# Optimization experiments

Measured on AMD Instinct MI355X. Metric: run time of the kernel, lower is better.

## Reference

```python
import jax, jax.numpy as jnp
import numpy as np

B, N, H = 8, 2000, 64  # batch, num_nodes(=input_dim), hidden(num_gru_units)


def _laplacian_self_loop(a):
    # batched: norm = D^{-1/2} (A + I) D^{-1/2}
    m = a + jnp.eye(a.shape[-1], dtype=a.dtype)
    d_inv_sqrt = jnp.sum(m, axis=-1) ** -0.5  # (B, N)
    return d_inv_sqrt[..., :, None] * m * d_inv_sqrt[..., None, :]


def _graph_conv(inputs, hidden_flat, adj, windd, W2, b2, W3, b3, W, b, out_dim):
    b_, _, n = inputs.shape
    # dynamic wind-based adjacency
    wind_now = inputs[:, 2, :] * 360.0  # (B, N)
    direction = jnp.abs(windd[None, :, :] - wind_now[:, :, None])  # (B, N, N)
    direction = jnp.where(direction > 360.0, 180.0, direction)
    d1 = jnp.maximum(jnp.cos(direction * (jnp.pi / 180.0)), 0.0)
    a = d1 @ W2.T + b2 + (adj @ W3.T + b3)[None]  # (B, N, N)
    a1 = _laplacian_self_loop(jnp.maximum(a, 0.0))
    # graph conv: concat [x, h] then A @ [.] then Linear
    x = jnp.concatenate([inputs[:, 0, :, None], hidden_flat.reshape(b_, n, H)], axis=2)  # (B,N,H+1)
    y = jnp.einsum('bij,bjh->bih', a1, x) @ W.T + b  # (B, N, out_dim)
    return y.reshape(b_, n * out_dim)


def reference(inputs, hidden_state, adj, windd, W2, b2, W3, b3, W1a, b1a, W1b, b1b, Wca1, Wca2, Wsa):
    b_, _, n = inputs.shape
    conc = _graph_conv(inputs, hidden_state, adj, windd, W2, b2, W3, b3, W1a, b1a, 2 * H)
    conc = conc.reshape(b_, 2 * H, n)  # faithful reshape (input_dim == N)
    # --- channel attention (CBAM) ---
    avg = jnp.mean(conc, axis=2, keepdims=True)  # (B, 2H, 1)
    mx = jnp.max(conc, axis=2, keepdims=True)
    def fc(v):
        return jnp.einsum('oc,bcx->box', Wca2, jax.nn.relu(jnp.einsum('oc,bcx->box', Wca1, v)))
    ca = jax.nn.sigmoid(fc(avg) + fc(mx))  # (B, 2H, 1)
    conc = ca * conc
    # --- spatial attention ---
    s = jnp.stack([jnp.mean(conc, axis=1), jnp.max(conc, axis=1)], axis=1)  # (B, 2, N)
    sa = jax.lax.conv_general_dilated(s, Wsa, window_strides=(1,), padding=((3, 3),),
                                      dimension_numbers=('NCH', 'OIH', 'NCH'))  # (B,1,N)
    conc = jax.nn.sigmoid(sa) * conc
    # --- GRU gates ---
    conc = jax.nn.sigmoid(conc.reshape(b_, 2 * H * n))
    r, u = jnp.split(conc, 2, axis=1)  # each (B, N*H)
    c = jnp.tanh(_graph_conv(inputs, r * hidden_state, adj, windd, W2, b2, W3, b3, W1b, b1b, H))
    new_hidden_state = u * hidden_state + (1.0 - u) * c
    return new_hidden_state


def setup_inputs() -> dict:
    key = jax.random.key(0)
    ks = jax.random.split(key, 12)
    inputs = jax.random.uniform(ks[0], (B, 3, N), dtype=jnp.float32)
    hidden_state = jax.random.normal(ks[1], (B, N * H), dtype=jnp.float32) * 0.1
    adj = jax.random.uniform(ks[2], (N, N), dtype=jnp.float32)
    windd = jax.random.uniform(ks[3], (N, N), dtype=jnp.float32) * 360.0
    sN = 1.0 / np.sqrt(N)
    W2 = jax.random.normal(ks[4], (N, N), dtype=jnp.float32) * sN
    b2 = jnp.zeros((N,), jnp.float32)
    W3 = jax.random.normal(ks[5], (N, N), dtype=jnp.float32) * sN
    b3 = jnp.zeros((N,), jnp.float32)
    sI = 1.0 / np.sqrt(H + 1)
    W1a = jax.random.normal(ks[6], (2 * H, H + 1), dtype=jnp.float32) * sI
    b1a = jnp.ones((2 * H,), jnp.float32)  # bias=1.0 in graph_conv1
    W1b = jax.random.normal(ks[7], (H, H + 1), dtype=jnp.float32) * sI
    b1b = jnp.zeros((H,), jnp.float32)
    Wca1 = jax.random.normal(ks[8], (2 * H // 16, 2 * H), dtype=jnp.float32) * (1.0 / np.sqrt(2 * H))
    Wca2 = jax.random.normal(ks[9], (2 * H, 2 * H // 16), dtype=jnp.float32) * (1.0 / np.sqrt(2 * H // 16))
    Wsa = jax.random.normal(ks[10], (1, 2, 7), dtype=jnp.float32) * (1.0 / np.sqrt(14))
    return {'inputs': inputs, 'hidden_state': hidden_state, 'adj': adj, 'windd': windd,
            'W2': W2, 'b2': b2, 'W3': W3, 'b3': b3, 'W1a': W1a, 'b1a': b1a,
            'W1b': W1b, 'b1b': b1b, 'Wca1': Wca1, 'Wca2': Wca2, 'Wsa': Wsa}
```

## Files before the change

kernel.cpp:

```cpp
#include <hip/hip_runtime.h>

#define NN 2000
#define BB 8
#define P  2048
#define NIT 32

typedef __attribute__((ext_vector_type(8))) short bf16x8;
typedef __attribute__((ext_vector_type(4))) float f32x4;

__device__ __forceinline__ float sigf(float x) { return 1.0f / (1.0f + expf(-x)); }

__device__ __forceinline__ short f2bf(float x) {
    union { float f; unsigned u; } v; v.f = x;
    unsigned r = v.u + 0x7fffu + ((v.u >> 16) & 1u);
    return (short)(r >> 16);
}
__device__ __forceinline__ float bf2f(short h) {
    union { unsigned u; float f; } v; v.u = ((unsigned)(unsigned short)h) << 16; return v.f;
}

__device__ __forceinline__ void gl2lds16(const short* g, short* l) {
    __builtin_amdgcn_global_load_lds(
        (const __attribute__((address_space(1))) void*)g,
        (__attribute__((address_space(3))) void*)l, 16, 0, 0);
}

__global__ __launch_bounds__(256) void k_cvt(
    const float* __restrict__ W2, const float* __restrict__ W3,
    const float* __restrict__ adj, const float* __restrict__ windd,
    const float* __restrict__ inputs,
    short* __restrict__ W2bf, short* __restrict__ W3bf,
    short* __restrict__ adjbf, short* __restrict__ d1bf)
{
    const int i = blockIdx.x, sel = blockIdx.y, t = threadIdx.x;
    const bool live = (i < NN) && (t < 250);
    if (sel < 3) {
        const float* s = (sel == 0) ? W2 : (sel == 1) ? W3 : adj;
        short* d = ((sel == 0) ? W2bf : (sel == 1) ? W3bf : adjbf) + ((size_t)i) * P + t * 8;
        bf16x8 v;
#pragma unroll
        for (int e = 0; e < 8; ++e) v[e] = 0;
        if (live) {
            const float* p = s + (size_t)i * NN + t * 8;
            float4 x0 = *(const float4*)p;
            float4 x1 = *(const float4*)(p + 4);
            float a[8] = {x0.x,x0.y,x0.z,x0.w,x1.x,x1.y,x1.z,x1.w};
#pragma unroll
            for (int e = 0; e < 8; ++e) v[e] = f2bf(a[e]);
        }
        *(bf16x8*)d = v;
    } else {
        const float DEG = 0.01745329251994329577f;
        float cw[8], sw[8];
        if (live) {
            const float* p = windd + (size_t)i * NN + t * 8;
            float4 x0 = *(const float4*)p;
            float4 x1 = *(const float4*)(p + 4);
            float a[8] = {x0.x,x0.y,x0.z,x0.w,x1.x,x1.y,x1.z,x1.w};
#pragma unroll
            for (int e = 0; e < 8; ++e) {
                float r = a[e] * DEG;
                cw[e] = __cosf(r);
                sw[e] = __sinf(r);
            }
        }
        __shared__ float cwn[8], swn[8];
        if (t < 8 && i < NN) {
            float wn = inputs[(size_t)t * 3 * NN + 2 * NN + i] * (360.0f * DEG);
            cwn[t] = __cosf(wn);
            swn[t] = __sinf(wn);
        }
        __syncthreads();
#pragma unroll
        for (int b = 0; b < BB; ++b) {
            bf16x8 v;
#pragma unroll
            for (int e = 0; e < 8; ++e) v[e] = 0;
            if (live) {
                const float cb_ = cwn[b], sb_ = swn[b];
#pragma unroll
                for (int e = 0; e < 8; ++e)
                    v[e] = f2bf(fmaxf(fmaf(cw[e], cb_, sw[e] * sb_), 0.0f));
            }
            *(bf16x8*)(d1bf + ((size_t)b * P + i) * P + t * 8) = v;
        }
    }
}

__global__ __launch_bounds__(512, 2) void k_gd(
    const short* __restrict__ d1bf, const short* __restrict__ W2bf,
    const float* __restrict__ b2, const short* __restrict__ adjw,
    short* __restrict__ m_bf, float* __restrict__ rowpart)
{
    __shared__ char smem[131072];
    const int t = threadIdx.x;
    const int w = t >> 6, lane = t & 63;
    const int wm = w >> 2, wn = w & 3;
    const int lr = lane & 15, lq = lane >> 4;
    const int tile = blockIdx.x;
    const int b = blockIdx.y;
    const int i0 = (tile & 7) * 256;
    const int j0 = (tile >> 3) * 256;
    const short* A  = d1bf + (size_t)b * P * P;
    const short* Bm = W2bf;

    const short* srcA[4];
    const short* srcB[4];
#pragma unroll
    for (int q = 0; q < 4; ++q) {
        const int c = q * 512 + t;
        const int r = c >> 3;
        const int g = (c & 7) ^ (r & 7);
        srcA[q] = A  + (size_t)(i0 + r) * P + g * 8;
        srcB[q] = Bm + (size_t)(j0 + r) * P + g * 8;
    }

#define STAGE_ALL(slot, ktI) do {                                                      \
        gl2lds16(srcA[0] + (ktI) * 64, (short*)(smem + (slot) * 32768 + (w * 64) * 16));          \
        gl2lds16(srcA[1] + (ktI) * 64, (short*)(smem + (slot) * 32768 + (512 + w * 64) * 16));    \
        gl2lds16(srcA[2] + (ktI) * 64, (short*)(smem + (slot) * 32768 + (1024 + w * 64) * 16));   \
        gl2lds16(srcA[3] + (ktI) * 64, (short*)(smem + (slot) * 32768 + (1536 + w * 64) * 16));   \
        gl2lds16(srcB[0] + (ktI) * 64, (short*)(smem + 65536 + (slot) * 32768 + (w * 64) * 16));          \
        gl2lds16(srcB[1] + (ktI) * 64, (short*)(smem + 65536 + (slot) * 32768 + (512 + w * 64) * 16));    \
        gl2lds16(srcB[2] + (ktI) * 64, (short*)(smem + 65536 + (slot) * 32768 + (1024 + w * 64) * 16));   \
        gl2lds16(srcB[3] + (ktI) * 64, (short*)(smem + 65536 + (slot) * 32768 + (1536 + w * 64) * 16)); } while (0)

    const int fx0 = (lq << 4) ^ ((lr & 7) << 4);
    const int fx1 = ((4 + lq) << 4) ^ ((lr & 7) << 4);
    const int arowB = (wm * 128 + lr) * 128;
    const int browB = (wn * 64 + lr) * 128;

    f32x4 acc[8][4];
#pragma unroll
    for (int m = 0; m < 8; ++m)
#pragma unroll
        for (int n = 0; n < 4; ++n) acc[m][n] = (f32x4){0.f, 0.f, 0.f, 0.f};
    bf16x8 aF[4][2], bF[4][2];

    STAGE_ALL(0, 0);
    asm volatile("s_waitcnt vmcnt(0)" ::: "memory");
    __builtin_amdgcn_s_barrier();
    asm volatile("" ::: "memory");

#define MFMA_(a_, b_, m, n) acc[m][n] = __builtin_amdgcn_mfma_f32_16x16x32_bf16(a_, b_, acc[m][n], 0, 0, 0)

    for (int kt = 0; kt < NIT; ++kt) {
        char* curA = smem + (kt & 1) * 32768;
        char* curB = smem + 65536 + (kt & 1) * 32768;
        const int stgSlot = (kt + 1) & 1;
        const int stgKt = (kt + 1 < NIT) ? (kt + 1) : (NIT - 1);

        STAGE_ALL(stgSlot, stgKt);

#pragma unroll
        for (int m = 0; m < 4; ++m) {
            aF[m][0] = *(const bf16x8*)(curA + arowB + m * 2048 + fx0);
            aF[m][1] = *(const bf16x8*)(curA + arowB + m * 2048 + fx1);
        }
#pragma unroll
        for (int n = 0; n < 4; ++n) {
            bF[n][0] = *(const bf16x8*)(curB + browB + n * 2048 + fx0);
            bF[n][1] = *(const bf16x8*)(curB + browB + n * 2048 + fx1);
        }
        asm volatile("s_waitcnt lgkmcnt(0)" ::: "memory");
        __builtin_amdgcn_sched_barrier(0);
        __builtin_amdgcn_s_setprio(1);
#pragma unroll
        for (int m = 0; m < 4; ++m)
#pragma unroll
            for (int n = 0; n < 4; ++n) {
                MFMA_(aF[m][0], bF[n][0], m, n);
                MFMA_(aF[m][1], bF[n][1], m, n);
            }
        __builtin_amdgcn_s_setprio(0);

#pragma unroll
        for (int m = 0; m < 4; ++m) {
            aF[m][0] = *(const bf16x8*)(curA + arowB + (m + 4) * 2048 + fx0);
            aF[m][1] = *(const bf16x8*)(curA + arowB + (m + 4) * 2048 + fx1);
        }
        asm volatile("s_waitcnt lgkmcnt(0)" ::: "memory");
        __builtin_amdgcn_sched_barrier(0);
        __builtin_amdgcn_s_setprio(1);
#pragma unroll
        for (int m = 0; m < 4; ++m)
#pragma unroll
            for (int n = 0; n < 4; ++n) {
                MFMA_(aF[m][0], bF[n][0], m + 4, n);
                MFMA_(aF[m][1], bF[n][1], m + 4, n);
            }
        __builtin_amdgcn_s_setprio(0);

        asm volatile("s_waitcnt vmcnt(0)" ::: "memory");
        __builtin_amdgcn_s_barrier();
        asm volatile("" ::: "memory");
    }

    const int rbase = i0 + wm * 128 + lq * 4;
    const int cbase = j0 + wn * 64 + lr;
    float* red = (float*)smem;
#pragma unroll
    for (int m = 0; m < 8; ++m) {
#pragma unroll
        for (int q = 0; q < 4; ++q) {
            const int row = rbase + m * 16 + q;
            float rs = 0.0f;
#pragma unroll
            for (int n = 0; n < 4; ++n) {
                const int col = cbase + n * 16;
                short o = 0;
                if (row < NN && col < NN) {
                    float x = acc[m][n][q] + b2[col] + bf2f(adjw[(size_t)row * NN + col]);
                    x = fmaxf(x, 0.0f);
                    if (row == col) x += 1.0f;
                    o = f2bf(x);
                    rs += x;
                }
                m_bf[((size_t)b * P + row) * P + col] = o;
            }
            red[(wm * 128 + m * 16 + lq * 4 + q) * 66 + (wn * 16 + lr)] = rs;
        }
    }
    __syncthreads();
    if (t < 256) {
        const float* rr = red + t * 66;
        float s = 0.0f;
#pragma unroll
        for (int k2 = 0; k2 < 64; ++k2) s += rr[k2];
        const int row = i0 + t;
        if (row < NN)
            rowpart[((size_t)b * 8 + (tile >> 3)) * 2048 + row] = s;
    }
#undef MFMA_
#undef STAGE_ALL
}

template<int EPI, int OUTD>
__global__ __launch_bounds__(256) void k_mfma(
    const short* __restrict__ Abase, const short* __restrict__ Bbase,
    const float* __restrict__ bias, const short* __restrict__ adjw,
    void* __restrict__ Cout, short* __restrict__ part, size_t aBatch)
{
    __shared__ short shA[4096];
    __shared__ short shB[4096];
    const int t = threadIdx.x;
    const int w = t >> 6, lane = t & 63;
    const int wr = w >> 1, wc = w & 1;

    int i0, j0, b, kt = 0;
    if (EPI == 2) {
        i0 = blockIdx.x * 128; j0 = 0; kt = blockIdx.y; b = blockIdx.z;
    } else {
        i0 = blockIdx.x * 128; j0 = blockIdx.y * 128; b = 0;
    }
    const int kb = (EPI == 2) ? kt * (P / 4) : 0;
    const int ke = (EPI == 2) ? kt * (P / 4) + (P / 4) : P;

    const short* A  = Abase + (size_t)b * aBatch;
    const short* Bm = Bbase + ((EPI == 2) ? (size_t)b * 128 * P : (size_t)0);

    f32x4 acc[4][4];
#pragma unroll
    for (int m = 0; m < 4; ++m)
#pragma unroll
        for (int n = 0; n < 4; ++n) acc[m][n] = (f32x4){0.f, 0.f, 0.f, 0.f};

    const int lidx0 = w * 128 + lane;
    const int lidx1 = lidx0 + 64;
    const short* aS0 = A  + (size_t)(i0 + (lidx0 >> 2)) * P + (lidx0 & 3) * 8;
    const short* aS1 = A  + (size_t)(i0 + (lidx1 >> 2)) * P + (lidx1 & 3) * 8;
    const short* bS0 = Bm + (size_t)(j0 + (lidx0 >> 2)) * P + (lidx0 & 3) * 8;
    const short* bS1 = Bm + (size_t)(j0 + (lidx1 >> 2)) * P + (lidx1 & 3) * 8;
    short* ldA0 = shA + (w * 128) * 8;
    short* ldA1 = shA + (w * 128 + 64) * 8;
    short* ldB0 = shB + (w * 128) * 8;
    short* ldB1 = shB + (w * 128 + 64) * 8;

    const int lr = lane & 15, lq = lane >> 4;
    const int aoff = (wr * 64 + lr) * 32 + lq * 8;
    const int boff = (wc * 64 + lr) * 32 + lq * 8;

    for (int k0 = kb; k0 < ke; k0 += 32) {
        gl2lds16(aS0 + k0, ldA0);
        gl2lds16(aS1 + k0, ldA1);
        gl2lds16(bS0 + k0, ldB0);
        gl2lds16(bS1 + k0, ldB1);
        __syncthreads();
        bf16x8 aF[4], bF[4];
#pragma unroll
        for (int m = 0; m < 4; ++m) aF[m] = *(const bf16x8*)(shA + aoff + m * 512);
#pragma unroll
        for (int n = 0; n < 4; ++n) bF[n] = *(const bf16x8*)(shB + boff + n * 512);
#pragma unroll
        for (int m = 0; m < 4; ++m)
#pragma unroll
            for (int n = 0; n < 4; ++n)
                acc[m][n] = __builtin_amdgcn_mfma_f32_16x16x32_bf16(aF[m], bF[n], acc[m][n], 0, 0, 0);
        __syncthreads();
    }

    const int rbase = i0 + wr * 64 + lq * 4;
    const int cbase = j0 + wc * 64 + lr;
#pragma unroll
    for (int m = 0; m < 4; ++m) {
#pragma unroll
        for (int n = 0; n < 4; ++n) {
            const int col = cbase + n * 16;
#pragma unroll
            for (int q = 0; q < 4; ++q) {
                const int row = rbase + m * 16 + q;
                float v = acc[m][n][q];
                if (EPI == 0) {
                    if (row < NN && col < NN)
                        ((short*)Cout)[(size_t)row * NN + col] = f2bf(v + bias[col]);
                } else {
                    if (row < NN && col < OUTD)
                        part[((size_t)(kt * BB + b) * NN + row) * OUTD + col] = f2bf(v);
                }
            }
        }
    }
}

__global__ __launch_bounds__(256) void k_combred(
    const short* __restrict__ part, const float* __restrict__ dinv,
    const float* __restrict__ bias, float* __restrict__ conc,
    float* __restrict__ avg, float* __restrict__ mx)
{
    const int c = blockIdx.x, b = blockIdx.y, t = threadIdx.x;
    const size_t S = (size_t)BB * NN * 128;
    const size_t base = (size_t)b * NN * 128;
    float sm = 0.0f, sx = -3.402823466e+38f;
    for (int n = t; n < NN; n += 256) {
        const size_t f = (size_t)c * NN + n;
        const int i = (int)(f >> 7), o = (int)(f & 127);
        const size_t pidx = base + f;
        float s = (bf2f(part[pidx]) + bf2f(part[pidx + S])) +
                  (bf2f(part[pidx + 2 * S]) + bf2f(part[pidx + 3 * S]));
        float v = s * dinv[b * NN + i] + bias[o];
        conc[pidx] = v;
        sm += v; sx = fmaxf(sx, v);
    }
#pragma unroll
    for (int off = 32; off > 0; off >>= 1) {
        sm += __shfl_down(sm, off);
        sx = fmaxf(sx, __shfl_down(sx, off));
    }
    __shared__ float rs[4], rm[4];
    if ((t & 63) == 0) { rs[t >> 6] = sm; rm[t >> 6] = sx; }
    __syncthreads();
    if (t == 0) {
        avg[b * 128 + c] = (rs[0] + rs[1] + rs[2] + rs[3]) * (1.0f / NN);
        mx[b * 128 + c]  = fmaxf(fmaxf(rm[0], rm[1]), fmaxf(rm[2], rm[3]));
    }
}

__global__ __launch_bounds__(256) void k_cfin(
    const short* __restrict__ part, const float* __restrict__ dinv,
    const float* __restrict__ bias, const float* __restrict__ u,
    const float* __restrict__ hidden, float* __restrict__ out)
{
    const size_t idx = (size_t)blockIdx.x * 256 + threadIdx.x;
    const size_t S = (size_t)BB * NN * 64;
    if (idx >= S) return;
    const int o = (int)(idx & 63);
    const size_t r = idx >> 6;
    const int i = (int)(r % NN);
    const int b = (int)(r / NN);
    float s = (bf2f(part[idx]) + bf2f(part[idx + S])) +
              (bf2f(part[idx + 2 * S]) + bf2f(part[idx + 3 * S]));
    float c = tanhf(s * dinv[b * NN + i] + bias[o]);
    float uu = u[idx];
    out[idx] = uu * hidden[idx] + (1.0f - uu) * c;
}

template<int OUT>
__global__ __launch_bounds__(128) void k_xwT(
    const float* __restrict__ inputs, const float* __restrict__ hsrc,
    const float* __restrict__ W, const float* __restrict__ rowpart,
    float* __restrict__ dinv, short* __restrict__ zT)
{
    const int b = blockIdx.y;
    const int j0 = blockIdx.x * 16;
    const int t = threadIdx.x;
    __shared__ float wl[128 * 65];
    __shared__ float xs[16 * 66];
    __shared__ float dj[16];
    for (int idx = t; idx < OUT * 65; idx += 128) wl[idx] = W[idx];
    for (int idx = t; idx < 16 * 64; idx += 128) {
        int jj = idx >> 6, hh = idx & 63, j = j0 + jj;
        xs[jj * 66 + 1 + hh] = (j < NN) ? hsrc[((size_t)b * NN + j) * 64 + hh] : 0.0f;
    }
    if (t < 16) {
        int j = j0 + t;
        xs[t * 66] = (j < NN) ? inputs[(size_t)b * 3 * NN + j] : 0.0f;
        float dv = 0.0f;
        if (j < NN) {
            if (OUT == 128) {
                float s = 0.0f;
#pragma unroll
                for (int jt = 0; jt < 8; ++jt)
                    s += rowpart[((size_t)b * 8 + jt) * 2048 + j];
                dv = rsqrtf(s);
                dinv[b * NN + j] = dv;
            } else {
                dv = dinv[b * NN + j];
            }
        }
        dj[t] = dv;
    }
    __syncthreads();
    for (int jj = 0; jj < 16; ++jj) {
        float a = 0.0f;
        if (t < OUT) {
            const float* xr = &xs[jj * 66];
            const float* wr = &wl[t * 65];
#pragma unroll
            for (int c = 0; c < 65; ++c) a = fmaf(xr[c], wr[c], a);
        }
        int j = j0 + jj;
        zT[((size_t)b * 128 + t) * P + j] = (t < OUT && j < NN) ? f2bf(a * dj[jj]) : (short)0;
    }
}

__global__ __launch_bounds__(256) void k_satgate(
    const float* __restrict__ conc, const float* __restrict__ avg,
    const float* __restrict__ mxv, const float* __restrict__ Wca1,
    const float* __restrict__ Wca2, const float* __restrict__ Wsa,
    const float* __restrict__ hidden, float* __restrict__ rh, float* __restrict__ u)
{
    const int b = blockIdx.y;
    const int n0 = blockIdx.x * 256;
    const int t = threadIdx.x;
    __shared__ float av[128], mv[128], h[16], cas[128];
    __shared__ float wsa[14];
    __shared__ float s0l[262], s1l[262];
    if (t < 128) { av[t] = avg[b * 128 + t]; mv[t] = mxv[b * 128 + t]; }
    if (t >= 128 && t < 142) wsa[t - 128] = Wsa[t - 128];
    __syncthreads();
    if (t < 16) {
        int o8 = t & 7;
        const float* src = (t < 8) ? av : mv;
        float s = 0.0f;
        for (int c = 0; c < 128; ++c) s = fmaf(Wca1[o8 * 128 + c], src[c], s);
        h[t] = fmaxf(s, 0.0f);
    }
    __syncthreads();
    if (t < 128) {
        float s = 0.0f;
#pragma unroll
        for (int k = 0; k < 8; ++k) s = fmaf(Wca2[t * 8 + k], h[k] + h[8 + k], s);
        cas[t] = sigf(s);
    }
    __syncthreads();

    const float* cb = conc + (size_t)b * NN * 128;
    {
        const int n = n0 + t;
        float sm = 0.0f, sx = -3.402823466e+38f;
        if (n < NN) {
            for (int c = 0; c < 128; ++c) {
                float v = cas[c] * cb[(size_t)c * NN + n];
                sm += v; sx = fmaxf(sx, v);
            }
            s0l[t + 3] = sm * (1.0f / 128.0f);
            s1l[t + 3] = sx;
        } else { s0l[t + 3] = 0.0f; s1l[t + 3] = 0.0f; }
    }
    if (t < 6) {
        const int hn = (t < 3) ? (n0 - 3 + t) : (n0 + 256 + (t - 3));
        const int hi = (t < 3) ? t : (256 + t);
        float sm = 0.0f, sx = -3.402823466e+38f;
        if (hn >= 0 && hn < NN) {
            for (int c = 0; c < 128; ++c) {
                float v = cas[c] * cb[(size_t)c * NN + hn];
                sm += v; sx = fmaxf(sx, v);
            }
            s0l[hi] = sm * (1.0f / 128.0f);
            s1l[hi] = sx;
        } else { s0l[hi] = 0.0f; s1l[hi] = 0.0f; }
    }
    __syncthreads();

    const int n = n0 + t;
    if (n >= NN) return;
    float sa = 0.0f;
#pragma unroll
    for (int k = 0; k < 7; ++k)
        sa += wsa[k] * s0l[t + k] + wsa[7 + k] * s1l[t + k];
    float gs = sigf(sa);
    for (int c = 0; c < 128; ++c) {
        float v = gs * cas[c] * cb[(size_t)c * NN + n];
        float g = sigf(v);
        if (c < 64)
            rh[(size_t)b * NN * 64 + (size_t)c * NN + n] =
                g * hidden[(size_t)b * NN * 64 + (size_t)c * NN + n];
        else
            u[(size_t)b * NN * 64 + (size_t)(c - 64) * NN + n] = g;
    }
}

extern "C" void kernel_launch(void* const* d_in, const int* in_sizes, int n_in,
                              void* d_out, int out_size, void* d_ws, size_t ws_size,
                              hipStream_t stream)
{
    (void)in_sizes; (void)n_in; (void)out_size; (void)ws_size;
    const float* inputs = (const float*)d_in[0];
    const float* hidden = (const float*)d_in[1];
    const float* adj    = (const float*)d_in[2];
    const float* windd  = (const float*)d_in[3];
    const float* W2     = (const float*)d_in[4];
    const float* b2     = (const float*)d_in[5];
    const float* W3     = (const float*)d_in[6];
    const float* b3     = (const float*)d_in[7];
    const float* W1a    = (const float*)d_in[8];
    const float* b1a    = (const float*)d_in[9];
    const float* W1b    = (const float*)d_in[10];
    const float* b1b    = (const float*)d_in[11];
    const float* Wca1   = (const float*)d_in[12];
    const float* Wca2   = (const float*)d_in[13];
    const float* Wsa    = (const float*)d_in[14];
    float* out = (float*)d_out;

    char* W = (char*)d_ws;
    short* adjW3bf = (short*)(W + 0);
    short* W2bf    = (short*)(W + 8000000);
    short* W3bf    = (short*)(W + 16388608);
    short* adjbf   = (short*)(W + 24777216);
    short* m_bf    = (short*)(W + 16388608);
    char* D = W + 83497472;
    short* d1bf = (short*)D;
    float* dinv = (float*)(D + 0);
    float* avgb = (float*)(D + 64000);
    float* mxb  = (float*)(D + 68096);
    short* zT   = (short*)(D + 204800);
    float* conc = (float*)(D + 4399104);
    float* rh   = (float*)(D + 12591104);
    float* ubuf = (float*)(D + 16687104);
    short* part = (short*)(D + 24879104);
    float* rowpart = (float*)(D + 67108864);

    const size_t PP = (size_t)P * P;

    k_cvt<<<dim3(P, 4), 256, 0, stream>>>(W2, W3, adj, windd, inputs,
                                          W2bf, W3bf, adjbf, d1bf);
    k_mfma<0, 0><<<dim3(16, 16, 1), 256, 0, stream>>>(adjbf, W3bf, b3, nullptr, adjW3bf, nullptr, 0);
    k_gd<<<dim3(64, BB), 512, 0, stream>>>(d1bf, W2bf, b2, adjW3bf, m_bf, rowpart);
    k_xwT<128><<<dim3(128, BB), 128, 0, stream>>>(inputs, hidden, W1a, rowpart, dinv, zT);
    k_mfma<2, 128><<<dim3(16, 4, BB), 256, 0, stream>>>(m_bf, zT, nullptr, nullptr, nullptr, part, PP);
    k_combred<<<dim3(128, BB), 256, 0, stream>>>(part, dinv, b1a, conc, avgb, mxb);
    k_satgate<<<dim3(8, BB), 256, 0, stream>>>(conc, avgb, mxb, Wca1, Wca2, Wsa, hidden, rh, ubuf);
    k_xwT<64><<<dim3(128, BB), 128, 0, stream>>>(inputs, rh, W1b, rowpart, dinv, zT);
    k_mfma<2, 64><<<dim3(16, 4, BB), 256, 0, stream>>>(m_bf, zT, nullptr, nullptr, nullptr, part, PP);
    k_cfin<<<(BB * NN * 64 + 255) / 256, 256, 0, stream>>>(part, dinv, b1b, ubuf, hidden, out);
}
```

Measured before the change: 396.5 us.

## Swizzle LDS layout in MFMA GEMM and add dedicated 64-wide aggregation kernel

```diff
diff --git a/kernel.cpp b/kernel.cpp
--- a/kernel.cpp
+++ b/kernel.cpp
@@ -235,10 +235,10 @@
 #undef STAGE_ALL
 }
 
-template<int EPI, int OUTD>
+template<int EPI>
 __global__ __launch_bounds__(256) void k_mfma(
     const short* __restrict__ Abase, const short* __restrict__ Bbase,
-    const float* __restrict__ bias, const short* __restrict__ adjw,
+    const float* __restrict__ bias,
     void* __restrict__ Cout, short* __restrict__ part, size_t aBatch)
 {
     __shared__ short shA[4096];
@@ -267,18 +267,22 @@
 
     const int lidx0 = w * 128 + lane;
     const int lidx1 = lidx0 + 64;
-    const short* aS0 = A  + (size_t)(i0 + (lidx0 >> 2)) * P + (lidx0 & 3) * 8;
-    const short* aS1 = A  + (size_t)(i0 + (lidx1 >> 2)) * P + (lidx1 & 3) * 8;
-    const short* bS0 = Bm + (size_t)(j0 + (lidx0 >> 2)) * P + (lidx0 & 3) * 8;
-    const short* bS1 = Bm + (size_t)(j0 + (lidx1 >> 2)) * P + (lidx1 & 3) * 8;
-    short* ldA0 = shA + (w * 128) * 8;
-    short* ldA1 = shA + (w * 128 + 64) * 8;
-    short* ldB0 = shB + (w * 128) * 8;
-    short* ldB1 = shB + (w * 128 + 64) * 8;
+    const int rA0 = lidx0 >> 2, rA1 = lidx1 >> 2;
+    const int gA0 = (lidx0 & 3) ^ ((lidx0 >> 3) & 3);
+    const int gA1 = (lidx1 & 3) ^ ((lidx1 >> 3) & 3);
+    const short* aS0 = A  + (size_t)(i0 + rA0) * P + gA0 * 8;
+    const short* aS1 = A  + (size_t)(i0 + rA1) * P + gA1 * 8;
+    const short* bS0 = Bm + (size_t)(j0 + rA0) * P + gA0 * 8;
+    const short* bS1 = Bm + (size_t)(j0 + rA1) * P + gA1 * 8;
+    short* ldA0 = shA + lidx0 * 8 - lane * 8 + lane * 8;
+    short* ldA1 = shA + lidx1 * 8;
+    short* ldB0 = shB + lidx0 * 8;
+    short* ldB1 = shB + lidx1 * 8;
 
     const int lr = lane & 15, lq = lane >> 4;
-    const int aoff = (wr * 64 + lr) * 32 + lq * 8;
-    const int boff = (wc * 64 + lr) * 32 + lq * 8;
+    const int axr = (lq ^ ((lr >> 1) & 3)) << 3;
+    const int aoff = (wr * 64 + lr) * 32 + axr;
+    const int boff = (wc * 64 + lr) * 32 + axr;
 
     for (int k0 = kb; k0 < ke; k0 += 32) {
         gl2lds16(aS0 + k0, ldA0);
@@ -314,9 +318,82 @@
                     if (row < NN && col < NN)
                         ((short*)Cout)[(size_t)row * NN + col] = f2bf(v + bias[col]);
                 } else {
-                    if (row < NN && col < OUTD)
-                        part[((size_t)(kt * BB + b) * NN + row) * OUTD + col] = f2bf(v);
+                    if (row < NN && col < 128)
+                        part[((size_t)(kt * BB + b) * NN + row) * 128 + col] = f2bf(v);
                 }
+            }
+        }
+    }
+}
+
+__global__ __launch_bounds__(256) void k_agg64(
+    const short* __restrict__ m_bf, const short* __restrict__ zT,
+    short* __restrict__ part)
+{
+    __shared__ short shA[4096];
+    __shared__ short shB[2048];
+    const int t = threadIdx.x;
+    const int w = t >> 6, lane = t & 63;
+    const int wr = w >> 1, wc = w & 1;
+    const int i0 = blockIdx.x * 128;
+    const int kt = blockIdx.y, b = blockIdx.z;
+    const int kb = kt * (P / 4), ke = kb + (P / 4);
+    const short* A  = m_bf + (size_t)b * P * P;
+    const short* Bm = zT + (size_t)b * 128 * P;
+
+    f32x4 acc[4][2];
+#pragma unroll
+    for (int m = 0; m < 4; ++m)
+#pragma unroll
+        for (int n = 0; n < 2; ++n) acc[m][n] = (f32x4){0.f, 0.f, 0.f, 0.f};
+
+    const int lidx0 = w * 128 + lane;
+    const int lidx1 = lidx0 + 64;
+    const int gA0 = (lidx0 & 3) ^ ((lidx0 >> 3) & 3);
+    const int gA1 = (lidx1 & 3) ^ ((lidx1 >> 3) & 3);
+    const int gB  = (t & 3) ^ ((t >> 3) & 3);
+    const short* aS0 = A  + (size_t)(i0 + (lidx0 >> 2)) * P + gA0 * 8;
+    const short* aS1 = A  + (size_t)(i0 + (lidx1 >> 2)) * P + gA1 * 8;
+    const short* bS  = Bm + (size_t)(t >> 2) * P + gB * 8;
+    short* ldA0 = shA + lidx0 * 8;
+    short* ldA1 = shA + lidx1 * 8;
+    short* ldB  = shB + t * 8;
+
+    const int lr = lane & 15, lq = lane >> 4;
+    const int axr = (lq ^ ((lr >> 1) & 3)) << 3;
+    const int aoff = (wr * 64 + lr) * 32 + axr;
+    const int boff = (wc * 32 + lr) * 32 + axr;
+
+    for (int k0 = kb; k0 < ke; k0 += 32) {
+        gl2lds16(aS0 + k0, ldA0);
+        gl2lds16(aS1 + k0, ldA1);
+        gl2lds16(bS + k0, ldB);
+        __syncthreads();
+        bf16x8 aF[4], bF[2];
+#pragma unroll
+        for (int m = 0; m < 4; ++m) aF[m] = *(const bf16x8*)(shA + aoff + m * 512);
+#pragma unroll
+        for (int n = 0; n < 2; ++n) bF[n] = *(const bf16x8*)(shB + boff + n * 512);
+#pragma unroll
+        for (int m = 0; m < 4; ++m)
+#pragma unroll
+            for (int n = 0; n < 2; ++n)
+                acc[m][n] = __builtin_amdgcn_mfma_f32_16x16x32_bf16(aF[m], bF[n], acc[m][n], 0, 0, 0);
+        __syncthreads();
+    }
+
+    const int rbase = i0 + wr * 64 + lq * 4;
+    const int cbase = wc * 32 + lr;
+#pragma unroll
+    for (int m = 0; m < 4; ++m) {
+#pragma unroll
+        for (int n = 0; n < 2; ++n) {
+            const int col = cbase + n * 16;
+#pragma unroll
+            for (int q = 0; q < 4; ++q) {
+                const int row = rbase + m * 16 + q;
+                if (row < NN)
+                    part[((size_t)(kt * BB + b) * NN + row) * 64 + col] = f2bf(acc[m][n][q]);
             }
         }
     }
@@ -544,13 +621,13 @@
 
     k_cvt<<<dim3(P, 4), 256, 0, stream>>>(W2, W3, adj, windd, inputs,
                                           W2bf, W3bf, adjbf, d1bf);
-    k_mfma<0, 0><<<dim3(16, 16, 1), 256, 0, stream>>>(adjbf, W3bf, b3, nullptr, adjW3bf, nullptr, 0);
+    k_mfma<0><<<dim3(16, 16, 1), 256, 0, stream>>>(adjbf, W3bf, b3, adjW3bf, nullptr, 0);
     k_gd<<<dim3(64, BB), 512, 0, stream>>>(d1bf, W2bf, b2, adjW3bf, m_bf, rowpart);
     k_xwT<128><<<dim3(128, BB), 128, 0, stream>>>(inputs, hidden, W1a, rowpart, dinv, zT);
-    k_mfma<2, 128><<<dim3(16, 4, BB), 256, 0, stream>>>(m_bf, zT, nullptr, nullptr, nullptr, part, PP);
+    k_mfma<2><<<dim3(16, 4, BB), 256, 0, stream>>>(m_bf, zT, nullptr, nullptr, part, PP);
     k_combred<<<dim3(128, BB), 256, 0, stream>>>(part, dinv, b1a, conc, avgb, mxb);
     k_satgate<<<dim3(8, BB), 256, 0, stream>>>(conc, avgb, mxb, Wca1, Wca2, Wsa, hidden, rh, ubuf);
     k_xwT<64><<<dim3(128, BB), 128, 0, stream>>>(inputs, rh, W1b, rowpart, dinv, zT);
-    k_mfma<2, 64><<<dim3(16, 4, BB), 256, 0, stream>>>(m_bf, zT, nullptr, nullptr, nullptr, part, PP);
+    k_agg64<<<dim3(16, 4, BB), 256, 0, stream>>>(m_bf, zT, part);
     k_cfin<<<(BB * NN * 64 + 255) / 256, 256, 0, stream>>>(part, dinv, b1b, ubuf, hidden, out);
 }
```

Result: faster. 388.0 us (-2.2%).
